# Performance work log

Hardware: AMD Instinct MI355X
Metric: run time of the kernel (lower is better)

Reference implementation:

```python
import jax, jax.numpy as jnp
import numpy as np

N_P, N_A, N_T = 20000, 10000, 5000
D_IN, D_OUT = 512, 256
E_P, E_A, E_T = 320000, 160000, 80000


def setup_inputs() -> dict:
    key = jax.random.key(0)
    ks = iter(jax.random.split(key, 64))

    def nrm(shape, scale=1.0):
        return jax.random.normal(next(ks), shape, dtype=jnp.float32) * scale

    def xav(shape):
        # xavier_uniform-like scale (gain 1.414), normal draw is fine for a baseline
        return nrm(shape, 1.414 * (2.0 / (shape[0] + shape[1])) ** 0.5)

    def edges(ne, n_src, n_dst):
        src = jax.random.randint(next(ks), (ne,), 0, n_src, dtype=jnp.int32)
        dst = jax.random.randint(next(ks), (ne,), 0, n_dst, dtype=jnp.int32)
        w = jax.random.uniform(next(ks), (ne,), dtype=jnp.float32) / 16.0  # ~normalized adj values
        return src, dst, w

    d = {}
    d["x_p"] = nrm((N_P, D_IN))
    d["x_a"] = nrm((N_A, D_IN))
    d["x_t"] = nrm((N_T, D_IN))
    d["e_p_a_src"], d["e_p_a_dst"], d["e_p_a_w"] = edges(E_P, N_A, N_P)
    d["e_p_t_src"], d["e_p_t_dst"], d["e_p_t_w"] = edges(E_P, N_T, N_P)
    d["e_a_p_src"], d["e_a_p_dst"], d["e_a_p_w"] = edges(E_A, N_P, N_A)
    d["e_a_t_src"], d["e_a_t_dst"], d["e_a_t_w"] = edges(E_A, N_T, N_A)
    d["e_t_p_src"], d["e_t_p_dst"], d["e_t_p_w"] = edges(E_T, N_P, N_T)
    d["e_t_a_src"], d["e_t_a_dst"], d["e_t_a_w"] = edges(E_T, N_A, N_T)
    # parameters for each target type k: W_proj per neighbor, w_self, w_share, w_att, w_cat, bias
    for k, nbs in (("p", ("a", "t")), ("a", ("p", "t")), ("t", ("p", "a"))):
        for nb in nbs:
            d[f"W_{k}_{nb}"] = xav((D_IN, D_OUT))
        d[f"ws_{k}"] = xav((D_IN, D_OUT))
        d[f"wsh_{k}"] = xav((D_OUT, D_OUT))
        d[f"watt_{k}"] = xav((2 * D_OUT, 1))
        d[f"wcat_{k}"] = xav((2 * D_OUT, D_OUT))
        d[f"b_{k}"] = xav((1, D_OUT))
    return d


def _hete_agg(x_self, w_self, w_share, w_att, w_cat, bias, nb_inputs):
    """nb_inputs: list of (x_nb, W_proj, src, dst, edge_w). Faithful to HeteAggregateLayer."""
    n = x_self.shape[0]
    self_ft = (x_self @ w_self) @ w_share  # [n, d]
    # per-relation: project -> spmm (gather + weighted segment-sum over dst) -> share
    nb_fts = [
        jax.ops.segment_sum((x_nb @ Wp)[src] * ew[:, None], dst, num_segments=n) @ w_share
        for (x_nb, Wp, src, dst, ew) in nb_inputs
    ]
    L = len(nb_fts)
    # e = leaky_relu(cat([cat(nb_ft,0), self_ft.repeat(L,1)],1) @ w_att)  -> [L*n, 1]
    e = jnp.concatenate(
        [jax.nn.leaky_relu(jnp.concatenate([f, self_ft], axis=1) @ w_att) for f in nb_fts],
        axis=0,
    )
    # NOTE: faithful replication of the original `e.view(-1, L)` reshape semantics
    att = jax.nn.softmax(e.reshape(n, L), axis=1)  # [n, L]
    agg = nb_fts[0] * att[:, 0:1]
    for i in range(1, L):
        agg = agg + nb_fts[i] * att[:, i : i + 1]
    return jnp.concatenate([agg, self_ft], axis=1) @ w_cat + bias


def reference(x_p, x_a, x_t,
              e_p_a_src, e_p_a_dst, e_p_a_w, e_p_t_src, e_p_t_dst, e_p_t_w,
              e_a_p_src, e_a_p_dst, e_a_p_w, e_a_t_src, e_a_t_dst, e_a_t_w,
              e_t_p_src, e_t_p_dst, e_t_p_w, e_t_a_src, e_t_a_dst, e_t_a_w,
              W_p_a, W_p_t, ws_p, wsh_p, watt_p, wcat_p, b_p,
              W_a_p, W_a_t, ws_a, wsh_a, watt_a, wcat_a, b_a,
              W_t_p, W_t_a, ws_t, wsh_t, watt_t, wcat_t, b_t):
    out_p = _hete_agg(x_p, ws_p, wsh_p, watt_p, wcat_p, b_p,
                      [(x_a, W_p_a, e_p_a_src, e_p_a_dst, e_p_a_w),
                       (x_t, W_p_t, e_p_t_src, e_p_t_dst, e_p_t_w)])
    out_a = _hete_agg(x_a, ws_a, wsh_a, watt_a, wcat_a, b_a,
                      [(x_p, W_a_p, e_a_p_src, e_a_p_dst, e_a_p_w),
                       (x_t, W_a_t, e_a_t_src, e_a_t_dst, e_a_t_w)])
    out_t = _hete_agg(x_t, ws_t, wsh_t, watt_t, wcat_t, b_t,
                      [(x_p, W_t_p, e_t_p_src, e_t_p_dst, e_t_p_w),
                       (x_a, W_t_a, e_t_a_src, e_t_a_dst, e_t_a_w)])
    return (out_p, out_a, out_t)
```

## Files before the change

### kernel.cpp

```cpp
#include <hip/hip_runtime.h>

namespace {

typedef short s16x8 __attribute__((ext_vector_type(8)));
typedef float f32x4 __attribute__((ext_vector_type(4)));

__device__ __forceinline__ float bf2f(unsigned short u) {
  return __uint_as_float(((unsigned)u) << 16);
}
__device__ __forceinline__ unsigned short f2bf(float f) {
  unsigned u = __float_as_uint(f);
  u += 0x7fffu + ((u >> 16) & 1u);
  return (unsigned short)(u >> 16);
}

struct Tc6 { const float* src[6]; unsigned short* dst[6]; int R[6]; };
__global__ __launch_bounds__(256) void transpose_cvt(Tc6 a) {
  int mat = blockIdx.z;
  int R = a.R[mat];
  int r0 = blockIdx.y * 32, c0 = blockIdx.x * 32;
  if (r0 >= R) return;
  const float* __restrict__ src = a.src[mat];
  unsigned short* __restrict__ dst = a.dst[mat];
  __shared__ float T[32][33];
  int tx = threadIdx.x & 31, ty = threadIdx.x >> 5;
  #pragma unroll
  for (int j = 0; j < 4; ++j) {
    int r = ty + j * 8;
    T[r][tx] = src[(size_t)(r0 + r) * 256 + c0 + tx];
  }
  __syncthreads();
  #pragma unroll
  for (int j = 0; j < 4; ++j) {
    int c = ty + j * 8;
    dst[(size_t)(c0 + c) * R + r0 + tx] = f2bf(T[tx][c]);
  }
}

struct Comb9 { const unsigned short* A[9]; const float* B[9]; unsigned short* C[9]; };
__global__ __launch_bounds__(256) void combine_mfma(Comb9 g) {
  int z = blockIdx.z;
  const unsigned short* __restrict__ A = g.A[z];
  const float* __restrict__ B = g.B[z];
  unsigned short* __restrict__ C = g.C[z];
  int row0 = blockIdx.y * 128;
  int col0 = blockIdx.x * 128;
  __shared__ unsigned short As[128 * 40];
  __shared__ unsigned short Bs[128 * 40];
  int tid = threadIdx.x, lane = tid & 63, w = tid >> 6;
  int quad = lane >> 4, m16 = lane & 15;
  f32x4 acc[2][8];
  #pragma unroll
  for (int r = 0; r < 2; ++r)
    #pragma unroll
    for (int c = 0; c < 8; ++c) acc[r][c] = (f32x4){0.f, 0.f, 0.f, 0.f};
  for (int k0 = 0; k0 < 256; k0 += 32) {
    #pragma unroll
    for (int i = 0; i < 2; ++i) {
      int ch = tid + i * 256;
      int m = ch >> 2, kk = (ch & 3) * 8;
      *(s16x8*)&As[m * 40 + kk] = *(const s16x8*)(A + (size_t)(row0 + m) * 256 + k0 + kk);
      const float4* bp = (const float4*)(B + (size_t)(col0 + m) * 256 + k0 + kk);
      float4 b0 = bp[0], b1 = bp[1];
      s16x8 bv;
      bv[0] = (short)f2bf(b0.x); bv[1] = (short)f2bf(b0.y);
      bv[2] = (short)f2bf(b0.z); bv[3] = (short)f2bf(b0.w);
      bv[4] = (short)f2bf(b1.x); bv[5] = (short)f2bf(b1.y);
      bv[6] = (short)f2bf(b1.z); bv[7] = (short)f2bf(b1.w);
      *(s16x8*)&Bs[m * 40 + kk] = bv;
    }
    __syncthreads();
    s16x8 af[2], bf[8];
    #pragma unroll
    for (int r = 0; r < 2; ++r)
      af[r] = *(const s16x8*)&As[(w * 32 + r * 16 + m16) * 40 + quad * 8];
    #pragma unroll
    for (int c = 0; c < 8; ++c)
      bf[c] = *(const s16x8*)&Bs[(c * 16 + m16) * 40 + quad * 8];
    #pragma unroll
    for (int r = 0; r < 2; ++r)
      #pragma unroll
      for (int c = 0; c < 8; ++c)
        acc[r][c] = __builtin_amdgcn_mfma_f32_16x16x32_bf16(af[r], bf[c], acc[r][c], 0, 0, 0);
    __syncthreads();
  }
  #pragma unroll
  for (int r = 0; r < 2; ++r)
    #pragma unroll
    for (int i = 0; i < 4; ++i) {
      int row = row0 + w * 32 + r * 16 + quad * 4 + i;
      #pragma unroll
      for (int c = 0; c < 8; ++c)
        C[(size_t)row * 512 + col0 + c * 16 + m16] = f2bf(acc[r][c][i]);
    }
}

struct Proj9 { const float* A[9]; const unsigned short* Bt[9]; unsigned short* C[9]; int M[9]; };
__global__ __launch_bounds__(256, 2) void proj_mfma9(Proj9 g) {
  int z = blockIdx.z;
  int M = g.M[z];
  int row0 = blockIdx.y * 64;
  if (row0 >= M) return;
  const float* __restrict__ A = g.A[z];
  const unsigned short* __restrict__ Bt = g.Bt[z];
  unsigned short* __restrict__ C = g.C[z];
  __shared__ unsigned short As[64 * 40];
  __shared__ unsigned short Bs[256 * 40];
  int tid = threadIdx.x, lane = tid & 63, w = tid >> 6;
  int quad = lane >> 4, m16 = lane & 15;
  f32x4 acc[16];
  #pragma unroll
  for (int c = 0; c < 16; ++c) acc[c] = (f32x4){0.f, 0.f, 0.f, 0.f};
  for (int k0 = 0; k0 < 512; k0 += 32) {
    {
      int m = tid >> 2, kk = (tid & 3) * 8;
      int gr = row0 + m;
      s16x8 v = {};
      if (gr < M) {
        const float4* ap = (const float4*)(A + (size_t)gr * 512 + k0 + kk);
        float4 a0 = ap[0], a1 = ap[1];
        v[0] = (short)f2bf(a0.x); v[1] = (short)f2bf(a0.y);
        v[2] = (short)f2bf(a0.z); v[3] = (short)f2bf(a0.w);
        v[4] = (short)f2bf(a1.x); v[5] = (short)f2bf(a1.y);
        v[6] = (short)f2bf(a1.z); v[7] = (short)f2bf(a1.w);
      }
      *(s16x8*)&As[m * 40 + kk] = v;
    }
    #pragma unroll
    for (int i = 0; i < 4; ++i) {
      int ch = tid + i * 256;
      int m = ch >> 2, kk = (ch & 3) * 8;
      *(s16x8*)&Bs[m * 40 + kk] = *(const s16x8*)(Bt + (size_t)m * 512 + k0 + kk);
    }
    __syncthreads();
    s16x8 af = *(const s16x8*)&As[(w * 16 + m16) * 40 + quad * 8];
    #pragma unroll
    for (int c = 0; c < 16; ++c) {
      s16x8 bf = *(const s16x8*)&Bs[(c * 16 + m16) * 40 + quad * 8];
      acc[c] = __builtin_amdgcn_mfma_f32_16x16x32_bf16(af, bf, acc[c], 0, 0, 0);
    }
    __syncthreads();
  }
  #pragma unroll
  for (int i = 0; i < 4; ++i) {
    int row = row0 + w * 16 + quad * 4 + i;
    if (row < M) {
      #pragma unroll
      for (int c = 0; c < 16; ++c)
        C[(size_t)row * 256 + c * 16 + m16] = f2bf(acc[c][i]);
    }
  }
}

struct Edges6 { const int* src[6]; const int* dst[6]; const float* w[6]; int nE[6]; int cbase[6]; };

__global__ __launch_bounds__(256) void hist_all(Edges6 ep, int* __restrict__ counts) {
  int rho = blockIdx.y;
  int e = blockIdx.x * 256 + threadIdx.x;
  if (e >= ep.nE[rho]) return;
  atomicAdd(&counts[ep.cbase[rho] + ep.dst[rho][e]], 1);
}

__global__ __launch_bounds__(256) void scan1(const int* __restrict__ cnt, int* __restrict__ out,
                                             int* __restrict__ part, int len) {
  __shared__ int sh[256];
  int base = blockIdx.x * 2048 + threadIdx.x * 8;
  int v[8];
  int s = 0;
  #pragma unroll
  for (int j = 0; j < 8; ++j) {
    int i = base + j;
    int x = (i < len) ? cnt[i] : 0;
    v[j] = s;
    s += x;
  }
  sh[threadIdx.x] = s;
  __syncthreads();
  for (int off = 1; off < 256; off <<= 1) {
    int t = (threadIdx.x >= off) ? sh[threadIdx.x - off] : 0;
    __syncthreads();
    sh[threadIdx.x] += t;
    __syncthreads();
  }
  int texcl = sh[threadIdx.x] - s;
  #pragma unroll
  for (int j = 0; j < 8; ++j) {
    int i = base + j;
    if (i < len) out[i] = texcl + v[j];
  }
  if (threadIdx.x == 255) part[blockIdx.x] = sh[255];
}

__global__ void scan2(int* __restrict__ part, int nb, int* __restrict__ total_out) {
  __shared__ int sh[64];
  int t = threadIdx.x;
  int v = (t < nb) ? part[t] : 0;
  sh[t] = v;
  __syncthreads();
  for (int off = 1; off < 64; off <<= 1) {
    int x = (t >= off) ? sh[t - off] : 0;
    __syncthreads();
    sh[t] += x;
    __syncthreads();
  }
  if (t < nb) part[t] = sh[t] - v;
  if (t == 63) *total_out = sh[63];
}

__global__ __launch_bounds__(256) void scan3(int* __restrict__ offs, int* __restrict__ cursor,
                                             const int* __restrict__ part, int len) {
  int i = blockIdx.x * 256 + threadIdx.x;
  if (i >= len) return;
  int v = offs[i] + part[i >> 11];
  offs[i] = v;
  cursor[i] = v;
}

__global__ __launch_bounds__(256) void fill_all(Edges6 ep, int* __restrict__ cursor,
                                                unsigned int* __restrict__ pay) {
  int rho = blockIdx.y;
  int e = blockIdx.x * 256 + threadIdx.x;
  if (e >= ep.nE[rho]) return;
  int pos = atomicAdd(&cursor[ep.cbase[rho] + ep.dst[rho][e]], 1);
  pay[pos] = (((unsigned)f2bf(ep.w[rho][e])) << 16) | (unsigned)ep.src[rho][e];
}

struct Gather6 { const unsigned short* proj[6]; unsigned short* out[6]; int cb[6]; int n[6]; };
__global__ __launch_bounds__(256) void gather_all(Gather6 g, const int* __restrict__ offs,
                                                  const unsigned int* __restrict__ pay) {
  int rho = blockIdx.y;
  int n = g.n[rho];
  int d = blockIdx.x * 4 + (threadIdx.x >> 6);
  if (d >= n) return;
  int lane = threadIdx.x & 63, half = lane >> 5, l32 = lane & 31;
  const unsigned short* __restrict__ proj = g.proj[rho];
  const int* of = offs + g.cb[rho];
  int s0 = of[d], s1 = of[d + 1];
  float acc[8] = {};
  int e = s0 + half;
  for (; e + 2 < s1; e += 4) {
    unsigned int u0 = pay[e], u1 = pay[e + 2];
    float wt0 = bf2f((unsigned short)(u0 >> 16));
    float wt1 = bf2f((unsigned short)(u1 >> 16));
    s16x8 v0 = *(const s16x8*)(proj + (size_t)(u0 & 0xffffu) * 256 + l32 * 8);
    s16x8 v1 = *(const s16x8*)(proj + (size_t)(u1 & 0xffffu) * 256 + l32 * 8);
    #pragma unroll
    for (int j = 0; j < 8; ++j) {
      acc[j] = fmaf(bf2f((unsigned short)v0[j]), wt0, acc[j]);
      acc[j] = fmaf(bf2f((unsigned short)v1[j]), wt1, acc[j]);
    }
  }
  if (e < s1) {
    unsigned int u = pay[e];
    float wt = bf2f((unsigned short)(u >> 16));
    s16x8 v = *(const s16x8*)(proj + (size_t)(u & 0xffffu) * 256 + l32 * 8);
    #pragma unroll
    for (int j = 0; j < 8; ++j) acc[j] = fmaf(bf2f((unsigned short)v[j]), wt, acc[j]);
  }
  #pragma unroll
  for (int j = 0; j < 8; ++j) acc[j] += __shfl(acc[j], lane ^ 32, 64);
  if (half == 0) {
    s16x8 o;
    #pragma unroll
    for (int j = 0; j < 8; ++j) o[j] = (short)f2bf(acc[j]);
    *(s16x8*)(g.out[rho] + (size_t)d * 256 + l32 * 8) = o;
  }
}

struct Att3 { const unsigned short* nb[3]; const unsigned short* self[3];
              const float* watt[3]; float* att[3]; int n[3]; };
__global__ __launch_bounds__(256) void e_att3(Att3 g) {
  int z = blockIdx.z;
  int n = g.n[z];
  int wv = threadIdx.x >> 6;
  int idx = blockIdx.x * 4 + wv;
  int lane = threadIdx.x & 63;
  __shared__ float ev[4];
  float sum = 0.f;
  if (idx < 2 * n) {
    int i = idx < n ? idx : idx - n;
    ushort4 v  = *(const ushort4*)(g.nb[z] + (size_t)idx * 256 + (lane << 2));
    ushort4 sv = *(const ushort4*)(g.self[z] + (size_t)i * 256 + (lane << 2));
    float4 wa = *(const float4*)(g.watt[z] + (lane << 2));
    float4 wb = *(const float4*)(g.watt[z] + 256 + (lane << 2));
    sum = bf2f(v.x) * wa.x + bf2f(v.y) * wa.y + bf2f(v.z) * wa.z + bf2f(v.w) * wa.w +
          bf2f(sv.x) * wb.x + bf2f(sv.y) * wb.y + bf2f(sv.z) * wb.z + bf2f(sv.w) * wb.w;
    #pragma unroll
    for (int off = 32; off > 0; off >>= 1) sum += __shfl_down(sum, off, 64);
  }
  if (lane == 0) ev[wv] = sum;
  __syncthreads();
  if (threadIdx.x < 2) {
    int base = blockIdx.x * 4 + threadIdx.x * 2;
    if (base < 2 * n) {
      float f0 = ev[threadIdx.x * 2], f1 = ev[threadIdx.x * 2 + 1];
      f0 = f0 > 0.f ? f0 : 0.01f * f0;
      f1 = f1 > 0.f ? f1 : 0.01f * f1;
      float m = fmaxf(f0, f1);
      float a = expf(f0 - m), b = expf(f1 - m);
      float inv = 1.f / (a + b);
      g.att[z][base] = a * inv;
      g.att[z][base + 1] = b * inv;
    }
  }
}

struct Fin3 { const unsigned short* nb[3]; const unsigned short* self[3]; const float* att[3];
              const unsigned short* Wt[3]; const float* bias[3]; float* out[3]; int M[3]; };
__global__ __launch_bounds__(256, 2) void final_mfma3(Fin3 g) {
  int z = blockIdx.z;
  int M = g.M[z];
  int row0 = blockIdx.y * 64;
  if (row0 >= M) return;
  const unsigned short* __restrict__ nbft = g.nb[z];
  const unsigned short* __restrict__ selfb = g.self[z];
  const float* __restrict__ att = g.att[z];
  const unsigned short* __restrict__ Wt = g.Wt[z];
  __shared__ unsigned short As[64 * 40];
  __shared__ unsigned short Bs[256 * 40];
  int tid = threadIdx.x, lane = tid & 63, w = tid >> 6;
  int quad = lane >> 4, m16 = lane & 15;
  f32x4 acc[16];
  #pragma unroll
  for (int c = 0; c < 16; ++c) acc[c] = (f32x4){0.f, 0.f, 0.f, 0.f};
  for (int k0 = 0; k0 < 512; k0 += 32) {
    {
      int m = tid >> 2, kk = (tid & 3) * 8;
      int gr = row0 + m;
      int kg = k0 + kk;
      s16x8 v = {};
      if (gr < M) {
        if (kg < 256) {
          float a0 = att[2 * gr], a1 = att[2 * gr + 1];
          s16x8 u0 = *(const s16x8*)(nbft + (size_t)gr * 256 + kg);
          s16x8 u1 = *(const s16x8*)(nbft + ((size_t)M + gr) * 256 + kg);
          #pragma unroll
          for (int j = 0; j < 8; ++j)
            v[j] = (short)f2bf(fmaf(a0, bf2f((unsigned short)u0[j]),
                                    a1 * bf2f((unsigned short)u1[j])));
        } else {
          v = *(const s16x8*)(selfb + (size_t)gr * 256 + (kg - 256));
        }
      }
      *(s16x8*)&As[m * 40 + kk] = v;
    }
    #pragma unroll
    for (int i = 0; i < 4; ++i) {
      int ch = tid + i * 256;
      int m = ch >> 2, kk = (ch & 3) * 8;
      *(s16x8*)&Bs[m * 40 + kk] = *(const s16x8*)(Wt + (size_t)m * 512 + k0 + kk);
    }
    __syncthreads();
    s16x8 af = *(const s16x8*)&As[(w * 16 + m16) * 40 + quad * 8];
    #pragma unroll
    for (int c = 0; c < 16; ++c) {
      s16x8 bf = *(const s16x8*)&Bs[(c * 16 + m16) * 40 + quad * 8];
      acc[c] = __builtin_amdgcn_mfma_f32_16x16x32_bf16(af, bf, acc[c], 0, 0, 0);
    }
    __syncthreads();
  }
  const float* __restrict__ bias = g.bias[z];
  float* __restrict__ out = g.out[z];
  #pragma unroll
  for (int i = 0; i < 4; ++i) {
    int row = row0 + w * 16 + quad * 4 + i;
    if (row < M) {
      #pragma unroll
      for (int c = 0; c < 16; ++c) {
        int col = c * 16 + m16;
        out[(size_t)row * 256 + col] = acc[c][i] + bias[col];
      }
    }
  }
}

}

extern "C" void kernel_launch(void* const* d_in, const int* in_sizes, int n_in,
                              void* d_out, int out_size, void* d_ws, size_t ws_size,
                              hipStream_t stream) {
  (void)in_sizes; (void)n_in; (void)out_size; (void)ws_size;
  const float* x[3] = {(const float*)d_in[0], (const float*)d_in[1], (const float*)d_in[2]};

  char* p = (char*)d_ws;
  unsigned short* projfull = (unsigned short*)p;  p += (size_t)105000 * 256 * 2;
  unsigned short* nbft = (unsigned short*)p;      p += (size_t)70000 * 256 * 2;
  unsigned short* wcatbt = (unsigned short*)p;    p += (size_t)3 * 256 * 512 * 2;
  int* offs = (int*)p;                            p += (size_t)70004 * 4;
  int* counts = (int*)p;                          p += (size_t)70000 * 4;
  int* part = (int*)p;                            p += 256;
  float* att_buf = (float*)p;                     p += (size_t)70000 * 4;
  unsigned int* csr_pay = (unsigned int*)p;       p += (size_t)1120000 * 4;
  unsigned short* wshT = nbft;
  unsigned short* Wcbt = (unsigned short*)((char*)nbft + 393216);

  const int n_of[3] = {20000, 10000, 5000};
  const int nbt[3][2] = {{1, 2}, {0, 2}, {0, 1}};
  const int ebase[3][2] = {{3, 6}, {9, 12}, {15, 18}};
  const int nE3[3] = {320000, 160000, 80000};
  const size_t out_off[3] = {0, (size_t)20000 * 256, (size_t)30000 * 256};
  const int tstart[3] = {0, 15000, 40000};
  const int selfoff[3] = {70000, 90000, 100000};
  const int nboff[3] = {0, 40000, 60000};

  Tc6 tc;
  for (int t = 0; t < 3; ++t) {
    tc.src[t] = (const float*)d_in[21 + t * 7 + 3];
    tc.dst[t] = wshT + (size_t)t * 256 * 256;
    tc.R[t] = 256;
    tc.src[3 + t] = (const float*)d_in[21 + t * 7 + 5];
    tc.dst[3 + t] = wcatbt + (size_t)t * 256 * 512;
    tc.R[3 + t] = 512;
  }
  transpose_cvt<<<dim3(8, 16, 6), 256, 0, stream>>>(tc);

  Comb9 c9;
  for (int t = 0; t < 3; ++t) {
    int wb = 21 + t * 7;
    for (int j = 0; j < 3; ++j) {
      int combo = t * 3 + j;
      c9.A[combo] = wshT + (size_t)t * 256 * 256;
      c9.B[combo] = (const float*)d_in[wb + j];
      c9.C[combo] = Wcbt + (size_t)combo * 256 * 512;
    }
  }
  combine_mfma<<<dim3(4, 2, 9), 256, 0, stream>>>(c9);

  Edges6 ep;
  const int cbase[6] = {0, 20000, 40000, 50000, 60000, 65000};
  for (int t = 0; t < 3; ++t)
    for (int r = 0; r < 2; ++r) {
      int rho = t * 2 + r, eb = ebase[t][r];
      ep.src[rho] = (const int*)d_in[eb];
      ep.dst[rho] = (const int*)d_in[eb + 1];
      ep.w[rho] = (const float*)d_in[eb + 2];
      ep.nE[rho] = nE3[t];
      ep.cbase[rho] = cbase[rho];
    }
  hipMemsetAsync(counts, 0, (size_t)70000 * 4, stream);
  hist_all<<<dim3(1250, 6), 256, 0, stream>>>(ep, counts);
  scan1<<<35, 256, 0, stream>>>(counts, offs, part, 70000);
  scan2<<<1, 64, 0, stream>>>(part, 35, offs + 70000);
  scan3<<<274, 256, 0, stream>>>(offs, counts, part, 70000);
  fill_all<<<dim3(1250, 6), 256, 0, stream>>>(ep, counts, csr_pay);

  Proj9 pj;
  for (int t = 0; t < 3; ++t) {
    int nb0 = nbt[t][0], nb1 = nbt[t][1];
    int m0 = n_of[nb0];
    pj.A[t * 3 + 0] = x[nb0];
    pj.C[t * 3 + 0] = projfull + (size_t)tstart[t] * 256;
    pj.M[t * 3 + 0] = m0;
    pj.A[t * 3 + 1] = x[nb1];
    pj.C[t * 3 + 1] = projfull + (size_t)(tstart[t] + m0) * 256;
    pj.M[t * 3 + 1] = n_of[nb1];
    pj.A[t * 3 + 2] = x[t];
    pj.C[t * 3 + 2] = projfull + (size_t)selfoff[t] * 256;
    pj.M[t * 3 + 2] = n_of[t];
    for (int j = 0; j < 3; ++j)
      pj.Bt[t * 3 + j] = Wcbt + (size_t)(t * 3 + j) * 256 * 512;
  }
  proj_mfma9<<<dim3(1, 313, 9), 256, 0, stream>>>(pj);

  Gather6 gt;
  for (int t = 0; t < 3; ++t) {
    int m0 = n_of[nbt[t][0]];
    for (int r = 0; r < 2; ++r) {
      int rho = t * 2 + r;
      gt.proj[rho] = projfull + (size_t)(tstart[t] + (r ? m0 : 0)) * 256;
      gt.out[rho] = nbft + (size_t)(nboff[t] + r * n_of[t]) * 256;
      gt.cb[rho] = cbase[rho];
      gt.n[rho] = n_of[t];
    }
  }
  gather_all<<<dim3(5000, 6), 256, 0, stream>>>(gt, offs, csr_pay);

  Att3 at;
  for (int t = 0; t < 3; ++t) {
    at.nb[t] = nbft + (size_t)nboff[t] * 256;
    at.self[t] = projfull + (size_t)selfoff[t] * 256;
    at.watt[t] = (const float*)d_in[21 + t * 7 + 4];
    at.att[t] = att_buf + nboff[t];
    at.n[t] = n_of[t];
  }
  e_att3<<<dim3(10000, 1, 3), 256, 0, stream>>>(at);

  Fin3 fn;
  for (int t = 0; t < 3; ++t) {
    fn.nb[t] = nbft + (size_t)nboff[t] * 256;
    fn.self[t] = projfull + (size_t)selfoff[t] * 256;
    fn.att[t] = att_buf + nboff[t];
    fn.Wt[t] = wcatbt + (size_t)t * 256 * 512;
    fn.bias[t] = (const float*)d_in[21 + t * 7 + 6];
    fn.out[t] = (float*)d_out + out_off[t];
    fn.M[t] = n_of[t];
  }
  final_mfma3<<<dim3(1, 313, 3), 256, 0, stream>>>(fn);
}
```

Baseline: 492.0 us.

## Prefetch next K-tile into registers and retile warps in projection and final GEMMs

The projection and final GEMM kernels now load the next K-slice of A and B from global memory into registers while MFMAs run on the current LDS tile, then write them to LDS after a barrier. The goal is to hide global load latency behind compute. Each wave now covers a 64x64 output tile (4x4 MFMAs) instead of 16 rows by 256 columns, which cuts LDS reads of B fragments per MFMA. Launch bounds are raised to 3 blocks per CU to allow more occupancy. This adds prefetch registers under a tighter register budget, which risks spills.

```diff
diff --git a/kernel.cpp b/kernel.cpp
--- a/kernel.cpp
+++ b/kernel.cpp
@@ -96,7 +96,7 @@
 }
 
 struct Proj9 { const float* A[9]; const unsigned short* Bt[9]; unsigned short* C[9]; int M[9]; };
-__global__ __launch_bounds__(256, 2) void proj_mfma9(Proj9 g) {
+__global__ __launch_bounds__(256, 3) void proj_mfma9(Proj9 g) {
   int z = blockIdx.z;
   int M = g.M[z];
   int row0 = blockIdx.y * 64;
@@ -108,48 +108,97 @@
   __shared__ unsigned short Bs[256 * 40];
   int tid = threadIdx.x, lane = tid & 63, w = tid >> 6;
   int quad = lane >> 4, m16 = lane & 15;
-  f32x4 acc[16];
-  #pragma unroll
-  for (int c = 0; c < 16; ++c) acc[c] = (f32x4){0.f, 0.f, 0.f, 0.f};
-  for (int k0 = 0; k0 < 512; k0 += 32) {
-    {
-      int m = tid >> 2, kk = (tid & 3) * 8;
-      int gr = row0 + m;
-      s16x8 v = {};
-      if (gr < M) {
-        const float4* ap = (const float4*)(A + (size_t)gr * 512 + k0 + kk);
-        float4 a0 = ap[0], a1 = ap[1];
-        v[0] = (short)f2bf(a0.x); v[1] = (short)f2bf(a0.y);
-        v[2] = (short)f2bf(a0.z); v[3] = (short)f2bf(a0.w);
-        v[4] = (short)f2bf(a1.x); v[5] = (short)f2bf(a1.y);
-        v[6] = (short)f2bf(a1.z); v[7] = (short)f2bf(a1.w);
-      }
-      *(s16x8*)&As[m * 40 + kk] = v;
-    }
+  int am = tid >> 2, akk = (tid & 3) * 8;
+  int gr = row0 + am;
+  f32x4 acc[4][4];
+  #pragma unroll
+  for (int r = 0; r < 4; ++r)
+    #pragma unroll
+    for (int c = 0; c < 4; ++c) acc[r][c] = (f32x4){0.f, 0.f, 0.f, 0.f};
+
+  float4 pa0 = {}, pa1 = {};
+  s16x8 pb[4];
+
+  if (gr < M) {
+    const float4* ap = (const float4*)(A + (size_t)gr * 512 + akk);
+    pa0 = ap[0]; pa1 = ap[1];
+  }
+  #pragma unroll
+  for (int i = 0; i < 4; ++i) {
+    int ch = tid + i * 256;
+    int m = ch >> 2, kk = (ch & 3) * 8;
+    pb[i] = *(const s16x8*)(Bt + (size_t)m * 512 + kk);
+  }
+  {
+    s16x8 v;
+    v[0] = (short)f2bf(pa0.x); v[1] = (short)f2bf(pa0.y);
+    v[2] = (short)f2bf(pa0.z); v[3] = (short)f2bf(pa0.w);
+    v[4] = (short)f2bf(pa1.x); v[5] = (short)f2bf(pa1.y);
+    v[6] = (short)f2bf(pa1.z); v[7] = (short)f2bf(pa1.w);
+    *(s16x8*)&As[am * 40 + akk] = v;
     #pragma unroll
     for (int i = 0; i < 4; ++i) {
       int ch = tid + i * 256;
       int m = ch >> 2, kk = (ch & 3) * 8;
-      *(s16x8*)&Bs[m * 40 + kk] = *(const s16x8*)(Bt + (size_t)m * 512 + k0 + kk);
-    }
-    __syncthreads();
-    s16x8 af = *(const s16x8*)&As[(w * 16 + m16) * 40 + quad * 8];
-    #pragma unroll
-    for (int c = 0; c < 16; ++c) {
-      s16x8 bf = *(const s16x8*)&Bs[(c * 16 + m16) * 40 + quad * 8];
-      acc[c] = __builtin_amdgcn_mfma_f32_16x16x32_bf16(af, bf, acc[c], 0, 0, 0);
-    }
-    __syncthreads();
-  }
-  #pragma unroll
-  for (int i = 0; i < 4; ++i) {
-    int row = row0 + w * 16 + quad * 4 + i;
-    if (row < M) {
+      *(s16x8*)&Bs[m * 40 + kk] = pb[i];
+    }
+  }
+  __syncthreads();
+
+  for (int k0 = 0; k0 < 512; k0 += 32) {
+    int kn = k0 + 32;
+    if (kn < 512) {
+      if (gr < M) {
+        const float4* ap = (const float4*)(A + (size_t)gr * 512 + kn + akk);
+        pa0 = ap[0]; pa1 = ap[1];
+      }
       #pragma unroll
-      for (int c = 0; c < 16; ++c)
-        C[(size_t)row * 256 + c * 16 + m16] = f2bf(acc[c][i]);
-    }
-  }
+      for (int i = 0; i < 4; ++i) {
+        int ch = tid + i * 256;
+        int m = ch >> 2, kk = (ch & 3) * 8;
+        pb[i] = *(const s16x8*)(Bt + (size_t)m * 512 + kn + kk);
+      }
+    }
+    s16x8 af[4], bf[4];
+    #pragma unroll
+    for (int r = 0; r < 4; ++r)
+      af[r] = *(const s16x8*)&As[(r * 16 + m16) * 40 + quad * 8];
+    #pragma unroll
+    for (int c = 0; c < 4; ++c)
+      bf[c] = *(const s16x8*)&Bs[(w * 64 + c * 16 + m16) * 40 + quad * 8];
+    #pragma unroll
+    for (int r = 0; r < 4; ++r)
+      #pragma unroll
+      for (int c = 0; c < 4; ++c)
+        acc[r][c] = __builtin_amdgcn_mfma_f32_16x16x32_bf16(af[r], bf[c], acc[r][c], 0, 0, 0);
+    __syncthreads();
+    if (kn < 512) {
+      s16x8 v;
+      v[0] = (short)f2bf(pa0.x); v[1] = (short)f2bf(pa0.y);
+      v[2] = (short)f2bf(pa0.z); v[3] = (short)f2bf(pa0.w);
+      v[4] = (short)f2bf(pa1.x); v[5] = (short)f2bf(pa1.y);
+      v[6] = (short)f2bf(pa1.z); v[7] = (short)f2bf(pa1.w);
+      *(s16x8*)&As[am * 40 + akk] = v;
+      #pragma unroll
+      for (int i = 0; i < 4; ++i) {
+        int ch = tid + i * 256;
+        int m = ch >> 2, kk = (ch & 3) * 8;
+        *(s16x8*)&Bs[m * 40 + kk] = pb[i];
+      }
+      __syncthreads();
+    }
+  }
+  #pragma unroll
+  for (int r = 0; r < 4; ++r)
+    #pragma unroll
+    for (int i = 0; i < 4; ++i) {
+      int row = row0 + r * 16 + quad * 4 + i;
+      if (row < M) {
+        #pragma unroll
+        for (int c = 0; c < 4; ++c)
+          C[(size_t)row * 256 + w * 64 + c * 16 + m16] = f2bf(acc[r][c][i]);
+      }
+    }
 }
 
 struct Edges6 { const int* src[6]; const int* dst[6]; const float* w[6]; int nE[6]; int cbase[6]; };
@@ -307,7 +356,7 @@
 
 struct Fin3 { const unsigned short* nb[3]; const unsigned short* self[3]; const float* att[3];
               const unsigned short* Wt[3]; const float* bias[3]; float* out[3]; int M[3]; };
-__global__ __launch_bounds__(256, 2) void final_mfma3(Fin3 g) {
+__global__ __launch_bounds__(256, 3) void final_mfma3(Fin3 g) {
   int z = blockIdx.z;
   int M = g.M[z];
   int row0 = blockIdx.y * 64;
@@ -320,58 +369,98 @@
   __shared__ unsigned short Bs[256 * 40];
   int tid = threadIdx.x, lane = tid & 63, w = tid >> 6;
   int quad = lane >> 4, m16 = lane & 15;
-  f32x4 acc[16];
-  #pragma unroll
-  for (int c = 0; c < 16; ++c) acc[c] = (f32x4){0.f, 0.f, 0.f, 0.f};
-  for (int k0 = 0; k0 < 512; k0 += 32) {
-    {
-      int m = tid >> 2, kk = (tid & 3) * 8;
-      int gr = row0 + m;
-      int kg = k0 + kk;
-      s16x8 v = {};
-      if (gr < M) {
-        if (kg < 256) {
-          float a0 = att[2 * gr], a1 = att[2 * gr + 1];
-          s16x8 u0 = *(const s16x8*)(nbft + (size_t)gr * 256 + kg);
-          s16x8 u1 = *(const s16x8*)(nbft + ((size_t)M + gr) * 256 + kg);
-          #pragma unroll
-          for (int j = 0; j < 8; ++j)
-            v[j] = (short)f2bf(fmaf(a0, bf2f((unsigned short)u0[j]),
-                                    a1 * bf2f((unsigned short)u1[j])));
-        } else {
-          v = *(const s16x8*)(selfb + (size_t)gr * 256 + (kg - 256));
-        }
-      }
-      *(s16x8*)&As[m * 40 + kk] = v;
-    }
+  int am = tid >> 2, akk = (tid & 3) * 8;
+  int gr = row0 + am;
+  float a0 = 0.f, a1 = 0.f;
+  if (gr < M) { a0 = att[2 * gr]; a1 = att[2 * gr + 1]; }
+  f32x4 acc[4][4];
+  #pragma unroll
+  for (int r = 0; r < 4; ++r)
+    #pragma unroll
+    for (int c = 0; c < 4; ++c) acc[r][c] = (f32x4){0.f, 0.f, 0.f, 0.f};
+
+  s16x8 pu0 = {}, pu1 = {};
+  s16x8 pb[4];
+
+  auto loadA = [&](int k0) {
+    int kg = k0 + akk;
+    if (gr < M) {
+      if (kg < 256) {
+        pu0 = *(const s16x8*)(nbft + (size_t)gr * 256 + kg);
+        pu1 = *(const s16x8*)(nbft + ((size_t)M + gr) * 256 + kg);
+      } else {
+        pu0 = *(const s16x8*)(selfb + (size_t)gr * 256 + (kg - 256));
+      }
+    }
+  };
+  auto loadB = [&](int k0) {
     #pragma unroll
     for (int i = 0; i < 4; ++i) {
       int ch = tid + i * 256;
       int m = ch >> 2, kk = (ch & 3) * 8;
-      *(s16x8*)&Bs[m * 40 + kk] = *(const s16x8*)(Wt + (size_t)m * 512 + k0 + kk);
-    }
-    __syncthreads();
-    s16x8 af = *(const s16x8*)&As[(w * 16 + m16) * 40 + quad * 8];
-    #pragma unroll
-    for (int c = 0; c < 16; ++c) {
-      s16x8 bf = *(const s16x8*)&Bs[(c * 16 + m16) * 40 + quad * 8];
-      acc[c] = __builtin_amdgcn_mfma_f32_16x16x32_bf16(af, bf, acc[c], 0, 0, 0);
-    }
-    __syncthreads();
+      pb[i] = *(const s16x8*)(Wt + (size_t)m * 512 + k0 + kk);
+    }
+  };
+  auto storeLDS = [&](int k0) {
+    int kg = k0 + akk;
+    s16x8 v = {};
+    if (gr < M) {
+      if (kg < 256) {
+        #pragma unroll
+        for (int j = 0; j < 8; ++j)
+          v[j] = (short)f2bf(fmaf(a0, bf2f((unsigned short)pu0[j]),
+                                  a1 * bf2f((unsigned short)pu1[j])));
+      } else {
+        v = pu0;
+      }
+    }
+    *(s16x8*)&As[am * 40 + akk] = v;
+    #pragma unroll
+    for (int i = 0; i < 4; ++i) {
+      int ch = tid + i * 256;
+      int m = ch >> 2, kk = (ch & 3) * 8;
+      *(s16x8*)&Bs[m * 40 + kk] = pb[i];
+    }
+  };
+
+  loadA(0); loadB(0); storeLDS(0);
+  __syncthreads();
+  for (int k0 = 0; k0 < 512; k0 += 32) {
+    int kn = k0 + 32;
+    if (kn < 512) { loadA(kn); loadB(kn); }
+    s16x8 af[4], bf[4];
+    #pragma unroll
+    for (int r = 0; r < 4; ++r)
+      af[r] = *(const s16x8*)&As[(r * 16 + m16) * 40 + quad * 8];
+    #pragma unroll
+    for (int c = 0; c < 4; ++c)
+      bf[c] = *(const s16x8*)&Bs[(w * 64 + c * 16 + m16) * 40 + quad * 8];
+    #pragma unroll
+    for (int r = 0; r < 4; ++r)
+      #pragma unroll
+      for (int c = 0; c < 4; ++c)
+        acc[r][c] = __builtin_amdgcn_mfma_f32_16x16x32_bf16(af[r], bf[c], acc[r][c], 0, 0, 0);
+    __syncthreads();
+    if (kn < 512) {
+      storeLDS(kn);
+      __syncthreads();
+    }
   }
   const float* __restrict__ bias = g.bias[z];
   float* __restrict__ out = g.out[z];
   #pragma unroll
-  for (int i = 0; i < 4; ++i) {
-    int row = row0 + w * 16 + quad * 4 + i;
-    if (row < M) {
-      #pragma unroll
-      for (int c = 0; c < 16; ++c) {
-        int col = c * 16 + m16;
-        out[(size_t)row * 256 + col] = acc[c][i] + bias[col];
-      }
-    }
-  }
+  for (int r = 0; r < 4; ++r)
+    #pragma unroll
+    for (int i = 0; i < 4; ++i) {
+      int row = row0 + r * 16 + quad * 4 + i;
+      if (row < M) {
+        #pragma unroll
+        for (int c = 0; c < 4; ++c) {
+          int col = w * 64 + c * 16 + m16;
+          out[(size_t)row * 256 + col] = acc[r][c][i] + bias[col];
+        }
+      }
+    }
 }
 
 }
```

New measurement: 479.1 us. -2.6%, faster.
